# Optimization experiments

Hardware: AMD Instinct MI355X
Metric: run time of the kernel (lower is better)

The kernel has to match this reference:

```python
import jax, jax.numpy as jnp
import numpy as np

N = 100_000   # nodes
E = 1_600_000 # edges (avg degree 16)
D = 128       # numeric_dim
H = 128       # hidden_dim
C = 2         # num_classes
EPS = 1e-5    # BatchNorm eps


def setup_inputs() -> dict:
    key = jax.random.key(0)
    ks = jax.random.split(key, 24)

    def lin(k, i, o):  # torch Linear init-ish, stored as [in, out]
        return (jax.random.normal(k, (i, o), jnp.float32) / np.sqrt(i)).astype(jnp.float32)

    inp = {
        "x": jax.random.normal(ks[0], (N, D), jnp.float32),
        "edge_index": jax.random.randint(ks[1], (2, E), 0, N),
        "in_w": lin(ks[2], D, H),
        "in_b": jnp.zeros((H,), jnp.float32),
        "cls_w": lin(ks[3], H, C),
        "cls_b": jnp.zeros((C,), jnp.float32),
    }
    k = 4
    for blk in ("b1", "b2", "b3"):
        inp[f"{blk}_lw"] = lin(ks[k + 0], H, H)      # SAGEConv lin_l (aggregated neighbors), has bias
        inp[f"{blk}_lb"] = jnp.zeros((H,), jnp.float32)
        inp[f"{blk}_rw"] = lin(ks[k + 1], H, H)      # SAGEConv lin_r (root), bias=False in PyG
        inp[f"{blk}_g"] = jnp.ones((H,), jnp.float32)   # BN gamma
        inp[f"{blk}_bt"] = jnp.zeros((H,), jnp.float32)  # BN beta
        k += 2
    return inp


def _sage_block(x, src, dst, lw, lb, rw, g, bt):
    # SAGEConv with mean aggregation: messages flow src -> dst
    agg = jax.ops.segment_sum(x[src], dst, num_segments=N)            # [N, H]
    deg = jax.ops.segment_sum(jnp.ones((src.shape[0], 1), x.dtype), dst, num_segments=N)
    mean = agg / jnp.maximum(deg, 1.0)
    out = mean @ lw + lb + x @ rw                                     # lin_l(mean) + lin_r(x)
    # BatchNorm1d (training-mode batch stats over nodes), biased variance
    mu = out.mean(axis=0)
    var = out.var(axis=0)
    out = (out - mu) * jax.lax.rsqrt(var + EPS) * g + bt
    out = jax.nn.relu(out)
    # dropout in eval mode = identity; skip is Identity (H == H)
    return out + x


def reference(x, edge_index, in_w, in_b, cls_w, cls_b,
              b1_lw, b1_lb, b1_rw, b1_g, b1_bt,
              b2_lw, b2_lb, b2_rw, b2_g, b2_bt,
              b3_lw, b3_lb, b3_rw, b3_g, b3_bt):
    src, dst = edge_index[0], edge_index[1]
    h = jax.nn.relu(x @ in_w + in_b)
    h = _sage_block(h, src, dst, b1_lw, b1_lb, b1_rw, b1_g, b1_bt)
    h = _sage_block(h, src, dst, b2_lw, b2_lb, b2_rw, b2_g, b2_bt)
    h = _sage_block(h, src, dst, b3_lw, b3_lb, b3_rw, b3_g, b3_bt)
    return h @ cls_w + cls_b  # [N, C] logits
```

## Files before the change

### kernel.cpp

```cpp
#include <hip/hip_runtime.h>

#define NN 100000
#define NE 1600000
#define HD 128
#define EPSI 1e-5f

using u32 = unsigned int;
using u16 = unsigned short;

typedef short bf16x8 __attribute__((ext_vector_type(8)));
typedef float f32x4  __attribute__((ext_vector_type(4)));
typedef u32   u32x4  __attribute__((ext_vector_type(4)));

constexpr int NRANGE      = 128;
constexpr int RSZ2        = 784;
constexpr int BINCAP      = 16384;
constexpr int PART_CHUNK4 = 1024;
constexpr int PART_GRID   = (NE / 4 + PART_CHUNK4 - 1) / PART_CHUNK4;

__device__ inline float bflo(u32 u) { return __uint_as_float(u << 16); }
__device__ inline float bfhi(u32 u) { return __uint_as_float(u & 0xFFFF0000u); }
__device__ inline u16 f2bf(float f) {
    u32 u = __float_as_uint(f);
    u += 0x7FFFu + ((u >> 16) & 1u);
    return (u16)(u >> 16);
}
__device__ inline u32 pack2(float a, float b) {
    return (u32)f2bf(a) | ((u32)f2bf(b) << 16);
}


__global__ __launch_bounds__(256) void k_part(const int* __restrict__ src,
                                              const int* __restrict__ dst,
                                              int* __restrict__ binCur,
                                              u32* __restrict__ binbuf) {
    __shared__ int hist[NRANGE], base[NRANGE], curs[NRANGE];
    const int t  = threadIdx.x;
    const int c0 = blockIdx.x * PART_CHUNK4;
    if (t < NRANGE) { hist[t] = 0; curs[t] = 0; }
    __syncthreads();

    int4 ds[4], ss[4];
    bool ok[4];
#pragma unroll
    for (int i = 0; i < 4; ++i) {
        const int c = c0 + t + 256 * i;
        ok[i] = c < NE / 4;
        if (ok[i]) {
            ds[i] = reinterpret_cast<const int4*>(dst)[c];
            ss[i] = reinterpret_cast<const int4*>(src)[c];
        }
    }
#pragma unroll
    for (int i = 0; i < 4; ++i) {
        if (ok[i]) {
            atomicAdd(&hist[ds[i].x / RSZ2], 1);
            atomicAdd(&hist[ds[i].y / RSZ2], 1);
            atomicAdd(&hist[ds[i].z / RSZ2], 1);
            atomicAdd(&hist[ds[i].w / RSZ2], 1);
        }
    }
    __syncthreads();
    if (t < NRANGE && hist[t] > 0) base[t] = atomicAdd(&binCur[t], hist[t]);
    __syncthreads();

#pragma unroll
    for (int i = 0; i < 4; ++i) {
        if (ok[i]) {
            const int d[4] = {ds[i].x, ds[i].y, ds[i].z, ds[i].w};
            const int s[4] = {ss[i].x, ss[i].y, ss[i].z, ss[i].w};
#pragma unroll
            for (int j = 0; j < 4; ++j) {
                const int r  = d[j] / RSZ2;
                const int ld = d[j] - r * RSZ2;
                const int p  = base[r] + atomicAdd(&curs[r], 1);
                if (p < BINCAP)
                    binbuf[(size_t)r * BINCAP + p] = ((u32)s[j] << 10) | (u32)ld;
            }
        }
    }
}

__global__ __launch_bounds__(1024) void k_fillL2(const int* __restrict__ binCur,
                                                 const u32* __restrict__ binbuf,
                                                 int* __restrict__ rp,
                                                 int* __restrict__ col) {
    __shared__ int hist[1024];
    __shared__ int sbuf[1024];
    __shared__ int bscan[NRANGE];
    const int b = blockIdx.x;
    const int t = threadIdx.x;

    hist[t] = 0;
    if (t < NRANGE) bscan[t] = min(binCur[t], BINCAP);
    __syncthreads();

    int bval = (t < NRANGE) ? bscan[t] : 0;
    for (int off = 1; off < NRANGE; off <<= 1) {
        const int o = (t >= off && t < NRANGE) ? bscan[t - off] : 0;
        __syncthreads();
        bval += o;
        if (t < NRANGE) bscan[t] = bval;
        __syncthreads();
    }
    const int binbase = (b == 0) ? 0 : bscan[b - 1];

    const int n = min(binCur[b], BINCAP);
    const u32* bin = binbuf + (size_t)b * BINCAP;
    for (int i = t; i < n; i += 1024)
        atomicAdd(&hist[bin[i] & 1023u], 1);
    __syncthreads();

    int v = hist[t];
    for (int off = 1; off < 1024; off <<= 1) {
        sbuf[t] = v;
        __syncthreads();
        if (t >= off) v += sbuf[t - off];
        __syncthreads();
    }
    const int excl = v - hist[t];
    const int rpv  = binbase + excl;
    const int idx  = b * RSZ2 + t;
    if (t < RSZ2 && idx < NN) rp[idx] = rpv;
    if (b == NRANGE - 1 && t == 0) rp[NN] = bscan[NRANGE - 1];
    __syncthreads();
    hist[t] = rpv;
    __syncthreads();

    for (int i = t; i < n; i += 1024) {
        const u32 e = bin[i];
        col[atomicAdd(&hist[e & 1023u], 1)] = (int)(e >> 10);
    }
}


struct WTArgs { const float* w[7]; u16* o[7]; };

__global__ void k_wt(WTArgs a) {
    const int m = blockIdx.y;
    const int n = blockIdx.x;
    const int k = threadIdx.x;
    a.o[m][n * HD + k] = f2bf(a.w[m][k * HD + n]);
}


__device__ inline void acc8(float* a, u32x4 v) {
    a[0] += bflo(v.x); a[1] += bfhi(v.x);
    a[2] += bflo(v.y); a[3] += bfhi(v.y);
    a[4] += bflo(v.z); a[5] += bfhi(v.z);
    a[6] += bflo(v.w); a[7] += bfhi(v.w);
}

__global__ __launch_bounds__(256) void k_agg(const u16* __restrict__ h,
                                             const int* __restrict__ rp,
                                             const int* __restrict__ col,
                                             u16* __restrict__ mean) {
    const int lane = threadIdx.x & 63;
    const int node = blockIdx.x * 4 + (threadIdx.x >> 6);
    const int grp  = lane >> 4;
    const int li   = lane & 15;
    const int r0 = rp[node], r1 = rp[node + 1];
    const size_t lof = (size_t)li * 8;
    float a[8];
#pragma unroll
    for (int i = 0; i < 8; ++i) a[i] = 0.f;
    int e = r0 + grp;
    for (; e + 12 < r1; e += 16) {
        const int s0 = col[e], s1 = col[e + 4], s2 = col[e + 8], s3 = col[e + 12];
        const u32x4 v0 = *reinterpret_cast<const u32x4*>(&h[(size_t)s0 * HD + lof]);
        const u32x4 v1 = *reinterpret_cast<const u32x4*>(&h[(size_t)s1 * HD + lof]);
        const u32x4 v2 = *reinterpret_cast<const u32x4*>(&h[(size_t)s2 * HD + lof]);
        const u32x4 v3 = *reinterpret_cast<const u32x4*>(&h[(size_t)s3 * HD + lof]);
        acc8(a, v0); acc8(a, v1); acc8(a, v2); acc8(a, v3);
    }
    for (; e < r1; e += 4) {
        const u32x4 v = *reinterpret_cast<const u32x4*>(&h[(size_t)col[e] * HD + lof]);
        acc8(a, v);
    }
#pragma unroll
    for (int i = 0; i < 8; ++i) {
        a[i] += __shfl_xor(a[i], 16);
        a[i] += __shfl_xor(a[i], 32);
    }
    if (lane < 16) {
        const float inv = 1.0f / fmaxf((float)(r1 - r0), 1.0f);
        u32x4 o;
        o.x = pack2(a[0] * inv, a[1] * inv);
        o.y = pack2(a[2] * inv, a[3] * inv);
        o.z = pack2(a[4] * inv, a[5] * inv);
        o.w = pack2(a[6] * inv, a[7] * inv);
        __builtin_nontemporal_store(o, reinterpret_cast<u32x4*>(&mean[(size_t)node * HD + lof]));
    }
}


template <int A1F32, int RELU, int STATS>
__global__ __launch_bounds__(256) void k_mgemm(
    const void* __restrict__ A1p, const u16* __restrict__ W1T,
    const u16* __restrict__ A2, const u16* __restrict__ W2T,
    const float* __restrict__ bias, u16* __restrict__ out,
    float* __restrict__ stats)
{
    __shared__ u32x4 Wlds[2048];
    const int t    = threadIdx.x;
    const int wv   = t >> 6;
    const int lane = t & 63;
    const int lid  = lane & 15;
    const int kseg = lane >> 4;
    const int row0 = blockIdx.x * 128 + wv * 32;

    f32x4 acc[2][8];
#pragma unroll
    for (int rf = 0; rf < 2; ++rf)
#pragma unroll
        for (int c = 0; c < 8; ++c) acc[rf][c] = (f32x4){0.f, 0.f, 0.f, 0.f};

    int  ar[2];
    bool rok[2];
#pragma unroll
    for (int rf = 0; rf < 2; ++rf) {
        ar[rf]  = row0 + rf * 16 + lid;
        rok[rf] = ar[rf] < NN;
    }

#pragma unroll
    for (int i = 0; i < 8; ++i) {
        const int g   = t + 256 * i;
        const int row = g >> 4;
        const int ch  = g & 15;
        Wlds[row * 16 + (ch ^ (row & 7))] = reinterpret_cast<const u32x4*>(W1T)[g];
    }
    u32x4 wreg[8];
    if (A2 != nullptr) {
#pragma unroll
        for (int i = 0; i < 8; ++i)
            wreg[i] = reinterpret_cast<const u32x4*>(W2T)[t + 256 * i];
    }

    bf16x8 af1[2][4], af2[2][4];
    if (A1F32) {
        const float* A = (const float*)A1p;
#pragma unroll
        for (int rf = 0; rf < 2; ++rf)
#pragma unroll
            for (int kk = 0; kk < 4; ++kk) {
                const int kof = kk * 32 + kseg * 8;
                if (rok[rf]) {
                    const float4 f0 = *reinterpret_cast<const float4*>(&A[(size_t)ar[rf] * HD + kof]);
                    const float4 f1 = *reinterpret_cast<const float4*>(&A[(size_t)ar[rf] * HD + kof + 4]);
                    af1[rf][kk][0] = (short)f2bf(f0.x); af1[rf][kk][1] = (short)f2bf(f0.y);
                    af1[rf][kk][2] = (short)f2bf(f0.z); af1[rf][kk][3] = (short)f2bf(f0.w);
                    af1[rf][kk][4] = (short)f2bf(f1.x); af1[rf][kk][5] = (short)f2bf(f1.y);
                    af1[rf][kk][6] = (short)f2bf(f1.z); af1[rf][kk][7] = (short)f2bf(f1.w);
                } else {
                    af1[rf][kk] = (bf16x8)0;
                }
            }
    } else {
        const u16* A = (const u16*)A1p;
#pragma unroll
        for (int rf = 0; rf < 2; ++rf)
#pragma unroll
            for (int kk = 0; kk < 4; ++kk) {
                const int kof = kk * 32 + kseg * 8;
                af1[rf][kk] = rok[rf]
                    ? *reinterpret_cast<const bf16x8*>(&A[(size_t)ar[rf] * HD + kof])
                    : (bf16x8)0;
            }
    }
    if (A2 != nullptr) {
#pragma unroll
        for (int rf = 0; rf < 2; ++rf)
#pragma unroll
            for (int kk = 0; kk < 4; ++kk) {
                const int kof = kk * 32 + kseg * 8;
                af2[rf][kk] = rok[rf]
                    ? *reinterpret_cast<const bf16x8*>(&A2[(size_t)ar[rf] * HD + kof])
                    : (bf16x8)0;
            }
    }

    __syncthreads();
#pragma unroll
    for (int kk = 0; kk < 4; ++kk) {
#pragma unroll
        for (int c = 0; c < 8; ++c) {
            const int brow = c * 16 + lid;
            const bf16x8 bf = *reinterpret_cast<const bf16x8*>(
                &Wlds[brow * 16 + ((kk * 4 + kseg) ^ (lid & 7))]);
#pragma unroll
            for (int rf = 0; rf < 2; ++rf)
                acc[rf][c] = __builtin_amdgcn_mfma_f32_16x16x32_bf16(af1[rf][kk], bf, acc[rf][c], 0, 0, 0);
        }
    }

    if (A2 != nullptr) {
        __syncthreads();
#pragma unroll
        for (int i = 0; i < 8; ++i) {
            const int g   = t + 256 * i;
            const int row = g >> 4;
            const int ch  = g & 15;
            Wlds[row * 16 + (ch ^ (row & 7))] = wreg[i];
        }
        __syncthreads();
#pragma unroll
        for (int kk = 0; kk < 4; ++kk) {
#pragma unroll
            for (int c = 0; c < 8; ++c) {
                const int brow = c * 16 + lid;
                const bf16x8 bf = *reinterpret_cast<const bf16x8*>(
                    &Wlds[brow * 16 + ((kk * 4 + kseg) ^ (lid & 7))]);
#pragma unroll
                for (int rf = 0; rf < 2; ++rf)
                    acc[rf][c] = __builtin_amdgcn_mfma_f32_16x16x32_bf16(af2[rf][kk], bf, acc[rf][c], 0, 0, 0);
            }
        }
    }

    float bv[8];
#pragma unroll
    for (int c = 0; c < 8; ++c) bv[c] = bias[c * 16 + lid];

    float sv[8], qv[8];
#pragma unroll
    for (int c = 0; c < 8; ++c) { sv[c] = 0.f; qv[c] = 0.f; }

#pragma unroll
    for (int rf = 0; rf < 2; ++rf) {
#pragma unroll
        for (int c = 0; c < 8; ++c) {
            const int colc = c * 16 + lid;
#pragma unroll
            for (int j = 0; j < 4; ++j) {
                const int rrow = row0 + rf * 16 + kseg * 4 + j;
                if (rrow < NN) {
                    float o = acc[rf][c][j] + bv[c];
                    if (RELU) o = fmaxf(o, 0.f);
                    out[(size_t)rrow * HD + colc] = f2bf(o);
                    sv[c] += o;
                    qv[c] += o * o;
                }
            }
        }
    }

    if constexpr (STATS) {
        __shared__ float ls[4][HD], lq[4][HD];
#pragma unroll
        for (int c = 0; c < 8; ++c) {
            sv[c] += __shfl_xor(sv[c], 16);
            sv[c] += __shfl_xor(sv[c], 32);
            qv[c] += __shfl_xor(qv[c], 16);
            qv[c] += __shfl_xor(qv[c], 32);
        }
        if (lane < 16) {
#pragma unroll
            for (int c = 0; c < 8; ++c) {
                ls[wv][c * 16 + lid] = sv[c];
                lq[wv][c * 16 + lid] = qv[c];
            }
        }
        __syncthreads();
        if (t < HD) {
            const float s = (ls[0][t] + ls[1][t]) + (ls[2][t] + ls[3][t]);
            atomicAdd(&stats[t], s);
        } else {
            const int j = t - HD;
            const float q = (lq[0][j] + lq[1][j]) + (lq[2][j] + lq[3][j]);
            atomicAdd(&stats[HD + j], q);
        }
    }
}


template <int CLS>
__global__ __launch_bounds__(256) void k_apply(
    const u16* __restrict__ outb, const float* __restrict__ stats,
    const float* __restrict__ g, const float* __restrict__ bt,
    u16* __restrict__ hb, const float* __restrict__ cw,
    const float* __restrict__ cb, float* __restrict__ logits)
{
    const int t = threadIdx.x;
    const size_t idx4 = (size_t)blockIdx.x * 256 + t;
    const int j = (int)(idx4 & 31) * 4;
    const float4 svv = *reinterpret_cast<const float4*>(&stats[j]);
    const float4 qvv = *reinterpret_cast<const float4*>(&stats[HD + j]);
    const float4 gv  = *reinterpret_cast<const float4*>(&g[j]);
    const float4 bv  = *reinterpret_cast<const float4*>(&bt[j]);
    const float invn = 1.0f / (float)NN;
    float sc[4], sh[4];
    {
        const float sa[4] = {svv.x, svv.y, svv.z, svv.w};
        const float qa[4] = {qvv.x, qvv.y, qvv.z, qvv.w};
        const float ga[4] = {gv.x, gv.y, gv.z, gv.w};
        const float ba[4] = {bv.x, bv.y, bv.z, bv.w};
#pragma unroll
        for (int i = 0; i < 4; ++i) {
            const float mean = sa[i] * invn;
            const float var  = qa[i] * invn - mean * mean;
            sc[i] = ga[i] * rsqrtf(var + EPSI);
            sh[i] = ba[i] - mean * sc[i];
        }
    }
    const uint2 o  = reinterpret_cast<const uint2*>(outb)[idx4];
    const uint2 hv = reinterpret_cast<const uint2*>(hb)[idx4];
    const float r0 = fmaxf(bflo(o.x) * sc[0] + sh[0], 0.f) + bflo(hv.x);
    const float r1 = fmaxf(bfhi(o.x) * sc[1] + sh[1], 0.f) + bfhi(hv.x);
    const float r2 = fmaxf(bflo(o.y) * sc[2] + sh[2], 0.f) + bflo(hv.y);
    const float r3 = fmaxf(bfhi(o.y) * sc[3] + sh[3], 0.f) + bfhi(hv.y);
    reinterpret_cast<uint2*>(hb)[idx4] = make_uint2(pack2(r0, r1), pack2(r2, r3));

    if constexpr (CLS) {
        const float4 w01 = *reinterpret_cast<const float4*>(&cw[j * 2]);
        const float4 w23 = *reinterpret_cast<const float4*>(&cw[j * 2 + 4]);
        float p0 = r0 * w01.x + r1 * w01.z + r2 * w23.x + r3 * w23.z;
        float p1 = r0 * w01.y + r1 * w01.w + r2 * w23.y + r3 * w23.w;
#pragma unroll
        for (int off = 1; off <= 16; off <<= 1) {
            p0 += __shfl_xor(p0, off);
            p1 += __shfl_xor(p1, off);
        }
        if ((t & 31) == 0) {
            const size_t row = idx4 >> 5;
            logits[row * 2 + 0] = p0 + cb[0];
            logits[row * 2 + 1] = p1 + cb[1];
        }
    }
}


extern "C" void kernel_launch(void* const* d_in, const int* in_sizes, int n_in,
                              void* d_out, int out_size, void* d_ws, size_t ws_size,
                              hipStream_t stream) {
    const float* x     = (const float*)d_in[0];
    const int*   ei    = (const int*)d_in[1];
    const float* in_w  = (const float*)d_in[2];
    const float* in_b  = (const float*)d_in[3];
    const float* cls_w = (const float*)d_in[4];
    const float* cls_b = (const float*)d_in[5];
    const float* blk_w[3][5];
    for (int bidx = 0; bidx < 3; ++bidx)
        for (int k = 0; k < 5; ++k)
            blk_w[bidx][k] = (const float*)d_in[6 + bidx * 5 + k];

    const int* src = ei;
    const int* dst = ei + NE;

    size_t off = 0;
    auto alloc = [&](size_t bytes) {
        void* p = (char*)d_ws + off;
        off += (bytes + 255) & ~(size_t)255;
        return p;
    };
    u16*   h      = (u16*)alloc((size_t)NN * HD * 2);
    u16*   tmp    = (u16*)alloc((size_t)NN * HD * 2);
    int*   rp     = (int*)alloc((size_t)(NN + 1) * 4);
    int*   col    = (int*)alloc((size_t)NE * 4);
    u16*   wtb    = (u16*)alloc((size_t)7 * HD * HD * 2);
    const size_t off_z = off;
    float* stats  = (float*)alloc((size_t)3 * 256 * 4);
    int*   binCur = (int*)alloc((size_t)NRANGE * 4);
    const size_t zspan = off - off_z;
    u32*   binbuf = (u32*)tmp;
    (void)ws_size; (void)n_in; (void)in_sizes; (void)out_size;

    (void)hipMemsetAsync(stats, 0, zspan, stream);

    WTArgs wa;
    wa.w[0] = in_w;
    for (int bidx = 0; bidx < 3; ++bidx) {
        wa.w[1 + bidx * 2] = blk_w[bidx][0];
        wa.w[2 + bidx * 2] = blk_w[bidx][2];
    }
    for (int m = 0; m < 7; ++m) wa.o[m] = wtb + (size_t)m * HD * HD;
    k_wt<<<dim3(HD, 7), HD, 0, stream>>>(wa);

    k_part<<<PART_GRID, 256, 0, stream>>>(src, dst, binCur, binbuf);
    k_fillL2<<<NRANGE, 1024, 0, stream>>>(binCur, binbuf, rp, col);

    const int gemm_grid  = (NN + 127) / 128;
    const int apply_grid = NN * 32 / 256;

    k_mgemm<1, 1, 0><<<gemm_grid, 256, 0, stream>>>(x, wtb, nullptr, nullptr, in_b, h, nullptr);

    for (int bidx = 0; bidx < 3; ++bidx) {
        const u16* lwT = wtb + (size_t)(1 + bidx * 2) * HD * HD;
        const u16* rwT = wtb + (size_t)(2 + bidx * 2) * HD * HD;
        const float* lb = blk_w[bidx][1];
        const float* g  = blk_w[bidx][3];
        const float* bt = blk_w[bidx][4];
        float* st = stats + bidx * 256;
        k_agg<<<NN / 4, 256, 0, stream>>>(h, rp, col, tmp);
        k_mgemm<0, 0, 1><<<gemm_grid, 256, 0, stream>>>(tmp, lwT, h, rwT, lb, tmp, st);
        if (bidx < 2)
            k_apply<0><<<apply_grid, 256, 0, stream>>>(tmp, st, g, bt, h,
                                                       nullptr, nullptr, nullptr);
        else
            k_apply<1><<<apply_grid, 256, 0, stream>>>(tmp, st, g, bt, h,
                                                       cls_w, cls_b, (float*)d_out);
    }
}
```

Measured before the change: 392.3 us.

## Gather neighbor features from an FP8 copy of h during aggregation

Keeps a second copy of the node features in FP8 (e4m3), written by a new conversion kernel after the input GEMM and by the apply kernel after each block. The neighbor aggregation then gathers 8-byte FP8 rows instead of 16-byte bf16 rows. This halves the bytes moved by the memory-bound random gather. In exchange it adds an extra write of the FP8 copy each layer and loses precision in the aggregated mean, which could push results past the accuracy tolerance. The FP8 path runs only when the workspace is large enough.

```diff
diff --git a/kernel.cpp b/kernel.cpp
--- a/kernel.cpp
+++ b/kernel.cpp
@@ -7,10 +7,12 @@
 
 using u32 = unsigned int;
 using u16 = unsigned short;
+using u8  = unsigned char;
 
 typedef short bf16x8 __attribute__((ext_vector_type(8)));
 typedef float f32x4  __attribute__((ext_vector_type(4)));
 typedef u32   u32x4  __attribute__((ext_vector_type(4)));
+typedef u32   u32x2  __attribute__((ext_vector_type(2)));
 
 constexpr int NRANGE      = 128;
 constexpr int RSZ2        = 784;
@@ -28,6 +30,52 @@
 __device__ inline u32 pack2(float a, float b) {
     return (u32)f2bf(a) | ((u32)f2bf(b) << 16);
 }
+
+#if __has_builtin(__builtin_amdgcn_cvt_pk_f32_fp8)
+typedef float fltx2 __attribute__((ext_vector_type(2)));
+__device__ inline void add4fp8(float* a, u32 w) {
+    const fltx2 lo = __builtin_amdgcn_cvt_pk_f32_fp8(w, false);
+    const fltx2 hi = __builtin_amdgcn_cvt_pk_f32_fp8(w, true);
+    a[0] += lo.x; a[1] += lo.y; a[2] += hi.x; a[3] += hi.y;
+}
+#else
+__device__ inline float fp8d(u32 b) {
+    const u32 em = b & 0x7Fu;
+    const u32 s  = (b & 0x80u) << 24;
+    if (em >= 8) return __uint_as_float(s | ((em << 20) + (120u << 23)));
+    const float f = (float)em * 0.001953125f;
+    return s ? -f : f;
+}
+__device__ inline void add4fp8(float* a, u32 w) {
+    a[0] += fp8d(w & 0xFFu);
+    a[1] += fp8d((w >> 8) & 0xFFu);
+    a[2] += fp8d((w >> 16) & 0xFFu);
+    a[3] += fp8d(w >> 24);
+}
+#endif
+
+#if __has_builtin(__builtin_amdgcn_cvt_pk_fp8_f32)
+__device__ inline u32 pk4fp8(float x0, float x1, float x2, float x3) {
+    u32 v = (u32)__builtin_amdgcn_cvt_pk_fp8_f32(x0, x1, 0, false);
+    v = (u32)__builtin_amdgcn_cvt_pk_fp8_f32(x2, x3, (int)v, true);
+    return v;
+}
+#else
+__device__ inline u32 f2fp8(float f) {
+    const u32 b = __float_as_uint(f);
+    const u32 s = (b >> 24) & 0x80u;
+    u32 v = b & 0x7FFFFFFFu;
+    if (v >= 0x43E00000u) return s | 0x7Eu;
+    if (v < (121u << 23)) return s;
+    u32 r = v - (120u << 23);
+    r = (r + 0x7FFFFu + ((r >> 20) & 1u)) >> 20;
+    if (r > 0x7Eu) r = 0x7Eu;
+    return s | r;
+}
+__device__ inline u32 pk4fp8(float x0, float x1, float x2, float x3) {
+    return f2fp8(x0) | (f2fp8(x1) << 8) | (f2fp8(x2) << 16) | (f2fp8(x3) << 24);
+}
+#endif
 
 
 __global__ __launch_bounds__(256) void k_part(const int* __restrict__ src,
@@ -141,6 +189,14 @@
     const int n = blockIdx.x;
     const int k = threadIdx.x;
     a.o[m][n * HD + k] = f2bf(a.w[m][k * HD + n]);
+}
+
+
+__global__ __launch_bounds__(256) void k_h8(const u16* __restrict__ h,
+                                            u32* __restrict__ h8w) {
+    const size_t idx = (size_t)blockIdx.x * 256 + threadIdx.x;
+    const uint2 v = reinterpret_cast<const uint2*>(h)[idx];
+    h8w[idx] = pk4fp8(bflo(v.x), bfhi(v.x), bflo(v.y), bfhi(v.y));
 }
 
 
@@ -190,6 +246,51 @@
         o.z = pack2(a[4] * inv, a[5] * inv);
         o.w = pack2(a[6] * inv, a[7] * inv);
         __builtin_nontemporal_store(o, reinterpret_cast<u32x4*>(&mean[(size_t)node * HD + lof]));
+    }
+}
+
+
+__global__ __launch_bounds__(256) void k_agg8(const u32* __restrict__ h8,
+                                              const int* __restrict__ rp,
+                                              const int* __restrict__ col,
+                                              u16* __restrict__ mean) {
+    const int lane = threadIdx.x & 63;
+    const int node = blockIdx.x * 4 + (threadIdx.x >> 6);
+    const int grp  = lane >> 4;
+    const int li   = lane & 15;
+    const int r0 = rp[node], r1 = rp[node + 1];
+    float a[8];
+#pragma unroll
+    for (int i = 0; i < 8; ++i) a[i] = 0.f;
+    int e = r0 + grp;
+    for (; e + 12 < r1; e += 16) {
+        const int s0 = col[e], s1 = col[e + 4], s2 = col[e + 8], s3 = col[e + 12];
+        const u32x2 v0 = *reinterpret_cast<const u32x2*>(&h8[(size_t)s0 * 32 + li * 2]);
+        const u32x2 v1 = *reinterpret_cast<const u32x2*>(&h8[(size_t)s1 * 32 + li * 2]);
+        const u32x2 v2 = *reinterpret_cast<const u32x2*>(&h8[(size_t)s2 * 32 + li * 2]);
+        const u32x2 v3 = *reinterpret_cast<const u32x2*>(&h8[(size_t)s3 * 32 + li * 2]);
+        add4fp8(a, v0.x); add4fp8(a + 4, v0.y);
+        add4fp8(a, v1.x); add4fp8(a + 4, v1.y);
+        add4fp8(a, v2.x); add4fp8(a + 4, v2.y);
+        add4fp8(a, v3.x); add4fp8(a + 4, v3.y);
+    }
+    for (; e < r1; e += 4) {
+        const u32x2 v = *reinterpret_cast<const u32x2*>(&h8[(size_t)col[e] * 32 + li * 2]);
+        add4fp8(a, v.x); add4fp8(a + 4, v.y);
+    }
+#pragma unroll
+    for (int i = 0; i < 8; ++i) {
+        a[i] += __shfl_xor(a[i], 16);
+        a[i] += __shfl_xor(a[i], 32);
+    }
+    if (lane < 16) {
+        const float inv = 1.0f / fmaxf((float)(r1 - r0), 1.0f);
+        u32x4 o;
+        o.x = pack2(a[0] * inv, a[1] * inv);
+        o.y = pack2(a[2] * inv, a[3] * inv);
+        o.z = pack2(a[4] * inv, a[5] * inv);
+        o.w = pack2(a[6] * inv, a[7] * inv);
+        __builtin_nontemporal_store(o, reinterpret_cast<u32x4*>(&mean[(size_t)node * HD + (size_t)li * 8]));
     }
 }
 
@@ -378,8 +479,9 @@
 __global__ __launch_bounds__(256) void k_apply(
     const u16* __restrict__ outb, const float* __restrict__ stats,
     const float* __restrict__ g, const float* __restrict__ bt,
-    u16* __restrict__ hb, const float* __restrict__ cw,
-    const float* __restrict__ cb, float* __restrict__ logits)
+    u16* __restrict__ hb, u32* __restrict__ h8w,
+    const float* __restrict__ cw, const float* __restrict__ cb,
+    float* __restrict__ logits)
 {
     const int t = threadIdx.x;
     const size_t idx4 = (size_t)blockIdx.x * 256 + t;
@@ -410,6 +512,8 @@
     const float r2 = fmaxf(bflo(o.y) * sc[2] + sh[2], 0.f) + bflo(hv.y);
     const float r3 = fmaxf(bfhi(o.y) * sc[3] + sh[3], 0.f) + bfhi(hv.y);
     reinterpret_cast<uint2*>(hb)[idx4] = make_uint2(pack2(r0, r1), pack2(r2, r3));
+    if (h8w != nullptr)
+        h8w[idx4] = pk4fp8(r0, r1, r2, r3);
 
     if constexpr (CLS) {
         const float4 w01 = *reinterpret_cast<const float4*>(&cw[j * 2]);
@@ -462,8 +566,10 @@
     float* stats  = (float*)alloc((size_t)3 * 256 * 4);
     int*   binCur = (int*)alloc((size_t)NRANGE * 4);
     const size_t zspan = off - off_z;
+    u32*   h8     = (u32*)alloc((size_t)NN * HD);
+    const bool useFp8 = (ws_size >= off);
     u32*   binbuf = (u32*)tmp;
-    (void)ws_size; (void)n_in; (void)in_sizes; (void)out_size;
+    (void)n_in; (void)in_sizes; (void)out_size;
 
     (void)hipMemsetAsync(stats, 0, zspan, stream);
 
@@ -483,6 +589,8 @@
     const int apply_grid = NN * 32 / 256;
 
     k_mgemm<1, 1, 0><<<gemm_grid, 256, 0, stream>>>(x, wtb, nullptr, nullptr, in_b, h, nullptr);
+    if (useFp8)
+        k_h8<<<apply_grid, 256, 0, stream>>>(h, h8);
 
     for (int bidx = 0; bidx < 3; ++bidx) {
         const u16* lwT = wtb + (size_t)(1 + bidx * 2) * HD * HD;
@@ -491,13 +599,20 @@
         const float* g  = blk_w[bidx][3];
         const float* bt = blk_w[bidx][4];
         float* st = stats + bidx * 256;
-        k_agg<<<NN / 4, 256, 0, stream>>>(h, rp, col, tmp);
+
+        if (useFp8)
+            k_agg8<<<NN / 4, 256, 0, stream>>>(h8, rp, col, tmp);
+        else
+            k_agg<<<NN / 4, 256, 0, stream>>>(h, rp, col, tmp);
+
         k_mgemm<0, 0, 1><<<gemm_grid, 256, 0, stream>>>(tmp, lwT, h, rwT, lb, tmp, st);
+
+        u32* h8out = (useFp8 && bidx < 2) ? h8 : nullptr;
         if (bidx < 2)
-            k_apply<0><<<apply_grid, 256, 0, stream>>>(tmp, st, g, bt, h,
+            k_apply<0><<<apply_grid, 256, 0, stream>>>(tmp, st, g, bt, h, h8out,
                                                        nullptr, nullptr, nullptr);
         else
-            k_apply<1><<<apply_grid, 256, 0, stream>>>(tmp, st, g, bt, h,
+            k_apply<1><<<apply_grid, 256, 0, stream>>>(tmp, st, g, bt, h, h8out,
                                                        cls_w, cls_b, (float*)d_out);
     }
 }
```

Result: faster. 370.0 us (-5.7%).
